# Kernel optimization log

Hardware: AMD Instinct MI355X
Metric: run time of the kernel (lower is better)

Reference implementation:

```python
import jax, jax.numpy as jnp
import numpy as np

D_K = 256.0  # K_dim from __init__, used only as 1/sqrt(d_k) scale


def setup_inputs() -> dict:
    key = jax.random.key(0)
    ks = jax.random.split(key, 8)
    B, S, L, DQ, DK, DV, H = 8, 4096, 64, 1024, 1024, 1024, 256
    Q = jax.random.normal(ks[0], (B, S, DQ), dtype=jnp.float32)
    K = jax.random.normal(ks[1], (L, DK), dtype=jnp.float32)
    V = jax.random.normal(ks[2], (B, S, DV), dtype=jnp.float32)
    attn_mask = jax.random.randint(ks[3], (B, S, 1), 0, 2).astype(jnp.bool_)
    Wq_w = jax.random.normal(ks[4], (H, DQ), dtype=jnp.float32) * 0.02
    Wq_b = jnp.zeros((H,), dtype=jnp.float32)
    Wk_w = jax.random.normal(ks[5], (H, DK), dtype=jnp.float32) * 0.02
    Wk_b = jnp.zeros((H,), dtype=jnp.float32)
    return {"Q": Q, "K": K, "V": V, "attn_mask": attn_mask,
            "Wq_w": Wq_w, "Wq_b": Wq_b, "Wk_w": Wk_w, "Wk_b": Wk_b}


def reference(Q, K, V, attn_mask, Wq_w, Wq_b, Wk_w, Wk_b):
    # Projections (the original's expand/repeat + mul + sum is exactly a GEMM)
    kh = K @ Wk_w.T + Wk_b                                  # (L, 256)
    qh = (Q @ Wq_w.T + Wq_b) / jnp.sqrt(jnp.float32(D_K))   # (B, S, 256)
    # S[b,s,l] = sum_d qh[b,s,d]*kh[l,d]; scores sums over labels too
    S = jnp.einsum('bsd,ld->bsl', qh, kh)                   # (B, S, L)
    scores = S.sum(-1)[..., None] + attn_mask.astype(jnp.float32) * (-1e9)  # (B,S,1)
    scores = jnp.swapaxes(scores, -1, -2)                   # (B, 1, S)
    attn = jax.nn.softmax(scores, axis=-1)                  # (B, 1, S)
    context = jnp.matmul(attn, V)[:, 0, :]                  # (B, DV)
    return context, attn
```

## Files before the change

kernel.cpp:

```cpp
#include <hip/hip_runtime.h>
#include <hip/hip_bf16.h>
#include <cstddef>


#define B 8
#define S 4096
#define DQ 1024
#define H 256
#define L 64
#define SCHUNK 32
#define NSCHUNK (S / SCHUNK)


__global__ void ksumc_kernel(const float* __restrict__ K, float* __restrict__ ks_c) {
    int c = blockIdx.x * 64 + threadIdx.x;
    float acc = 0.f;
#pragma unroll 8
    for (int l = 0; l < L; ++l) acc += K[l * DQ + c];
    ks_c[c] = acc;
}

__global__ void ksum_kernel(const float* __restrict__ Wk_w, const float* __restrict__ Wk_b,
                            const float* __restrict__ ks_c, float* __restrict__ ksum) {
    __shared__ float sv[DQ];
    for (int i = threadIdx.x; i < DQ; i += 256) sv[i] = ks_c[i];
    __syncthreads();
    int wave = threadIdx.x >> 6, lane = threadIdx.x & 63;
    int d = blockIdx.x * 4 + wave;
    const float* wr = Wk_w + (size_t)d * DQ;
    float acc = 0.f;
#pragma unroll
    for (int j = 0; j < 4; ++j) {
        int idx = j * 256 + lane * 4;
        float4 a = *(const float4*)(wr + idx);
        float4 b = *(const float4*)(sv + idx);
        acc += a.x * b.x + a.y * b.y + a.z * b.z + a.w * b.w;
    }
    for (int off = 32; off; off >>= 1) acc += __shfl_down(acc, off);
    if (lane == 0) ksum[d] = acc + 64.f * Wk_b[d];
}

__global__ void wvec_bias_kernel(const float* __restrict__ Wq_w, const float* __restrict__ Wq_b,
                                 const float* __restrict__ ksum, float* __restrict__ w,
                                 float* __restrict__ bias) {
    __shared__ float ks[H];
    __shared__ float red[4][64];
    __shared__ float red2[4];
    ks[threadIdx.x] = ksum[threadIdx.x];
    __syncthreads();
    int wave = threadIdx.x >> 6, lane = threadIdx.x & 63;
    if (blockIdx.x < 16) {
        int c = blockIdx.x * 64 + lane;
        float acc = 0.f;
#pragma unroll 8
        for (int j = 0; j < 64; ++j) {
            int d = wave + 4 * j;
            acc += Wq_w[(size_t)d * DQ + c] * ks[d];
        }
        red[wave][lane] = acc;
        __syncthreads();
        if (wave == 0)
            w[c] = (red[0][lane] + red[1][lane] + red[2][lane] + red[3][lane]) * 0.0625f;
    } else {
        float v = Wq_b[threadIdx.x] * ks[threadIdx.x];
        for (int off = 32; off; off >>= 1) v += __shfl_down(v, off);
        if (lane == 0) red2[wave] = v;
        __syncthreads();
        if (threadIdx.x == 0)
            bias[0] = (red2[0] + red2[1] + red2[2] + red2[3]) * 0.0625f;
    }
}

__global__ void fused_main_kernel(const float* __restrict__ Q, const float* __restrict__ V,
                                  const float* __restrict__ w, const float* __restrict__ bias,
                                  const int* __restrict__ mask,
                                  float* __restrict__ escore, float* __restrict__ partial) {
    int sc = blockIdx.x, b = blockIdx.y;
    __shared__ float sw[DQ];
    __shared__ float es[SCHUNK];
    for (int i = threadIdx.x; i < DQ; i += 256) sw[i] = w[i];
    float sb = bias[0];
    __syncthreads();
    int wave = threadIdx.x >> 6, lane = threadIdx.x & 63;
#pragma unroll
    for (int r = 0; r < 8; ++r) {
        int row = sc * SCHUNK + wave * 8 + r;
        const float* q = Q + ((size_t)b * S + row) * DQ;
        float acc = 0.f;
#pragma unroll
        for (int j = 0; j < 4; ++j) {
            int idx = j * 256 + lane * 4;
            float4 qv = *(const float4*)(q + idx);
            float4 wv = *(const float4*)(sw + idx);
            acc += qv.x * wv.x + qv.y * wv.y + qv.z * wv.z + qv.w * wv.w;
        }
        for (int off = 32; off; off >>= 1) acc += __shfl_down(acc, off);
        if (lane == 0) {
            float e = mask[(size_t)b * S + row] ? 0.f : __expf(acc + sb);
            es[wave * 8 + r] = e;
            escore[(size_t)b * S + row] = e;
        }
    }
    __syncthreads();
    const float* vb = V + ((size_t)b * S + (size_t)sc * SCHUNK) * DQ + threadIdx.x * 4;
    float4 acc4 = {0.f, 0.f, 0.f, 0.f};
#pragma unroll 8
    for (int s = 0; s < SCHUNK; ++s) {
        float a = es[s];
        float4 v = *(const float4*)(vb + (size_t)s * DQ);
        acc4.x += a * v.x; acc4.y += a * v.y; acc4.z += a * v.z; acc4.w += a * v.w;
    }
    *(float4*)(partial + ((size_t)b * NSCHUNK + sc) * DQ + threadIdx.x * 4) = acc4;
}

__global__ void denom_kernel(const float* __restrict__ escore, float* __restrict__ inv) {
    int b = blockIdx.x;
    __shared__ float red[4];
    int wave = threadIdx.x >> 6, lane = threadIdx.x & 63;
    float lsum = 0.f;
    for (int i = threadIdx.x; i < S; i += 256) lsum += escore[(size_t)b * S + i];
    for (int off = 32; off; off >>= 1) lsum += __shfl_down(lsum, off);
    if (lane == 0) red[wave] = lsum;
    __syncthreads();
    if (threadIdx.x == 0) inv[b] = 1.0f / (red[0] + red[1] + red[2] + red[3]);
}

__global__ void epilogue_kernel(const float* __restrict__ escore, const float* __restrict__ partial,
                                const float* __restrict__ inv,
                                float* __restrict__ ctx, float* __restrict__ attn) {
    if (blockIdx.x < 128) {
        int i = blockIdx.x * 256 + threadIdx.x;
        attn[i] = escore[i] * inv[i >> 12];
    } else {
        int idx = (blockIdx.x - 128) * 256 + threadIdx.x;
        int b = idx >> 10, d = idx & 1023;
        const float* p = partial + (size_t)b * NSCHUNK * DQ + d;
        float acc = 0.f;
#pragma unroll 8
        for (int sc = 0; sc < NSCHUNK; ++sc) acc += p[(size_t)sc * DQ];
        ctx[idx] = acc * inv[b];
    }
}

extern "C" void kernel_launch(void* const* d_in, const int* in_sizes, int n_in,
                              void* d_out, int out_size, void* d_ws, size_t ws_size,
                              hipStream_t stream) {
    const float* Q    = (const float*)d_in[0];
    const float* K    = (const float*)d_in[1];
    const float* V    = (const float*)d_in[2];
    const int*   mask = (const int*)d_in[3];
    const float* Wq_w = (const float*)d_in[4];
    const float* Wq_b = (const float*)d_in[5];
    const float* Wk_w = (const float*)d_in[6];
    const float* Wk_b = (const float*)d_in[7];

    float* ws     = (float*)d_ws;
    float* ks_c   = ws;
    float* ksum   = ws + 1024;
    float* wv     = ws + 1280;
    float* bias   = ws + 2304;
    float* inv    = ws + 2312;
    float* escore = ws + 4096;
    float* partial = ws + 4096 + B * S;

    float* ctx  = (float*)d_out;
    float* attn = (float*)d_out + B * DQ;

    ksumc_kernel<<<16, 64, 0, stream>>>(K, ks_c);
    ksum_kernel<<<H / 4, 256, 0, stream>>>(Wk_w, Wk_b, ks_c, ksum);
    wvec_bias_kernel<<<17, 256, 0, stream>>>(Wq_w, Wq_b, ksum, wv, bias);
    fused_main_kernel<<<dim3(NSCHUNK, B), 256, 0, stream>>>(Q, V, wv, bias, mask, escore, partial);
    denom_kernel<<<B, 256, 0, stream>>>(escore, inv);
    epilogue_kernel<<<160, 256, 0, stream>>>(escore, partial, inv, ctx, attn);
}
```

Before: 313.8 us.

## Split fused main kernel into scores and context kernels with atomic denominator

Replaces the fused score-plus-V kernel with two kernels. The first computes masked exp scores for 16 rows per block, issuing all row loads up front with a shared-memory reduction, and accumulates the softmax denominator with atomics, which removes the separate denom kernel. The second reads V in chunks of 16 rows with batched loads to raise memory-level parallelism. The cost is an extra launch, an extra pass over escore, twice as many partial rows for the epilogue to reduce, and a memset.

```diff
diff --git a/kernel.cpp b/kernel.cpp
--- a/kernel.cpp
+++ b/kernel.cpp
@@ -8,8 +8,9 @@
 #define DQ 1024
 #define H 256
 #define L 64
-#define SCHUNK 32
-#define NSCHUNK (S / SCHUNK)
+#define RPB 16
+#define SC2 16
+#define NSC2 (S / SC2)
 
 
 __global__ void ksumc_kernel(const float* __restrict__ K, float* __restrict__ ks_c) {
@@ -71,74 +72,86 @@
     }
 }
 
-__global__ void fused_main_kernel(const float* __restrict__ Q, const float* __restrict__ V,
-                                  const float* __restrict__ w, const float* __restrict__ bias,
-                                  const int* __restrict__ mask,
-                                  float* __restrict__ escore, float* __restrict__ partial) {
-    int sc = blockIdx.x, b = blockIdx.y;
-    __shared__ float sw[DQ];
-    __shared__ float es[SCHUNK];
-    for (int i = threadIdx.x; i < DQ; i += 256) sw[i] = w[i];
-    float sb = bias[0];
+__global__ __launch_bounds__(256) void scores_kernel(
+        const float* __restrict__ Q, const float* __restrict__ w,
+        const float* __restrict__ bias, const int* __restrict__ mask,
+        float* __restrict__ escore, float* __restrict__ denom) {
+    int t = threadIdx.x;
+    size_t base = (size_t)blockIdx.x * RPB;
+    float4 wv = *(const float4*)(w + t * 4);
+    __shared__ float sp[RPB * 256];
+    __shared__ float bsum[RPB];
+    const float* qb = Q + base * DQ + t * 4;
+
+    float4 qv[RPB];
+#pragma unroll
+    for (int r = 0; r < RPB; ++r) qv[r] = *(const float4*)(qb + (size_t)r * DQ);
+#pragma unroll
+    for (int r = 0; r < RPB; ++r)
+        sp[r * 256 + t] = qv[r].x * wv.x + qv[r].y * wv.y + qv[r].z * wv.z + qv[r].w * wv.w;
     __syncthreads();
-    int wave = threadIdx.x >> 6, lane = threadIdx.x & 63;
+
+    int r = t >> 4, j = t & 15;
+    float s = 0.f;
 #pragma unroll
-    for (int r = 0; r < 8; ++r) {
-        int row = sc * SCHUNK + wave * 8 + r;
-        const float* q = Q + ((size_t)b * S + row) * DQ;
-        float acc = 0.f;
+    for (int k = 0; k < 16; ++k) s += sp[r * 256 + k * 16 + j];
+    s += __shfl_xor(s, 8, 64);
+    s += __shfl_xor(s, 4, 64);
+    s += __shfl_xor(s, 2, 64);
+    s += __shfl_xor(s, 1, 64);
+    if (j == 0) {
+        size_t row = base + r;
+        float e = mask[row] ? 0.f : __expf(s + bias[0]);
+        escore[row] = e;
+        bsum[r] = e;
+    }
+    __syncthreads();
+    if (t == 0) {
+        float d0 = 0.f;
 #pragma unroll
-        for (int j = 0; j < 4; ++j) {
-            int idx = j * 256 + lane * 4;
-            float4 qv = *(const float4*)(q + idx);
-            float4 wv = *(const float4*)(sw + idx);
-            acc += qv.x * wv.x + qv.y * wv.y + qv.z * wv.z + qv.w * wv.w;
-        }
-        for (int off = 32; off; off >>= 1) acc += __shfl_down(acc, off);
-        if (lane == 0) {
-            float e = mask[(size_t)b * S + row] ? 0.f : __expf(acc + sb);
-            es[wave * 8 + r] = e;
-            escore[(size_t)b * S + row] = e;
+        for (int k = 0; k < RPB; ++k) d0 += bsum[k];
+        atomicAdd(denom + (base >> 12), d0);
+    }
+}
+
+__global__ __launch_bounds__(256) void ctx_partial_kernel(
+        const float* __restrict__ V, const float* __restrict__ escore,
+        float* __restrict__ partial) {
+    int sc = blockIdx.x, b = blockIdx.y, t = threadIdx.x;
+    __shared__ float es[SC2];
+    if (t < SC2) es[t] = escore[(size_t)b * S + sc * SC2 + t];
+    __syncthreads();
+    const float* vb = V + ((size_t)b * S + (size_t)sc * SC2) * DQ + t * 4;
+    float4 acc = {0.f, 0.f, 0.f, 0.f};
+#pragma unroll
+    for (int s0 = 0; s0 < SC2; s0 += 8) {
+        float4 v[8];
+#pragma unroll
+        for (int k = 0; k < 8; ++k) v[k] = *(const float4*)(vb + (size_t)(s0 + k) * DQ);
+#pragma unroll
+        for (int k = 0; k < 8; ++k) {
+            float a = es[s0 + k];
+            acc.x += a * v[k].x; acc.y += a * v[k].y;
+            acc.z += a * v[k].z; acc.w += a * v[k].w;
         }
     }
-    __syncthreads();
-    const float* vb = V + ((size_t)b * S + (size_t)sc * SCHUNK) * DQ + threadIdx.x * 4;
-    float4 acc4 = {0.f, 0.f, 0.f, 0.f};
-#pragma unroll 8
-    for (int s = 0; s < SCHUNK; ++s) {
-        float a = es[s];
-        float4 v = *(const float4*)(vb + (size_t)s * DQ);
-        acc4.x += a * v.x; acc4.y += a * v.y; acc4.z += a * v.z; acc4.w += a * v.w;
-    }
-    *(float4*)(partial + ((size_t)b * NSCHUNK + sc) * DQ + threadIdx.x * 4) = acc4;
-}
-
-__global__ void denom_kernel(const float* __restrict__ escore, float* __restrict__ inv) {
-    int b = blockIdx.x;
-    __shared__ float red[4];
-    int wave = threadIdx.x >> 6, lane = threadIdx.x & 63;
-    float lsum = 0.f;
-    for (int i = threadIdx.x; i < S; i += 256) lsum += escore[(size_t)b * S + i];
-    for (int off = 32; off; off >>= 1) lsum += __shfl_down(lsum, off);
-    if (lane == 0) red[wave] = lsum;
-    __syncthreads();
-    if (threadIdx.x == 0) inv[b] = 1.0f / (red[0] + red[1] + red[2] + red[3]);
+    *(float4*)(partial + ((size_t)b * NSC2 + sc) * DQ + t * 4) = acc;
 }
 
 __global__ void epilogue_kernel(const float* __restrict__ escore, const float* __restrict__ partial,
-                                const float* __restrict__ inv,
+                                const float* __restrict__ denom,
                                 float* __restrict__ ctx, float* __restrict__ attn) {
     if (blockIdx.x < 128) {
         int i = blockIdx.x * 256 + threadIdx.x;
-        attn[i] = escore[i] * inv[i >> 12];
+        attn[i] = escore[i] / denom[i >> 12];
     } else {
         int idx = (blockIdx.x - 128) * 256 + threadIdx.x;
         int b = idx >> 10, d = idx & 1023;
-        const float* p = partial + (size_t)b * NSCHUNK * DQ + d;
+        const float* p = partial + (size_t)b * NSC2 * DQ + d;
         float acc = 0.f;
 #pragma unroll 8
-        for (int sc = 0; sc < NSCHUNK; ++sc) acc += p[(size_t)sc * DQ];
-        ctx[idx] = acc * inv[b];
+        for (int sc = 0; sc < NSC2; ++sc) acc += p[(size_t)sc * DQ];
+        ctx[idx] = acc / denom[b];
     }
 }
 
@@ -159,17 +172,18 @@
     float* ksum   = ws + 1024;
     float* wv     = ws + 1280;
     float* bias   = ws + 2304;
-    float* inv    = ws + 2312;
+    float* denom  = ws + 2312;
     float* escore = ws + 4096;
     float* partial = ws + 4096 + B * S;
 
     float* ctx  = (float*)d_out;
     float* attn = (float*)d_out + B * DQ;
 
+    hipMemsetAsync(denom, 0, B * sizeof(float), stream);
     ksumc_kernel<<<16, 64, 0, stream>>>(K, ks_c);
     ksum_kernel<<<H / 4, 256, 0, stream>>>(Wk_w, Wk_b, ks_c, ksum);
     wvec_bias_kernel<<<17, 256, 0, stream>>>(Wq_w, Wq_b, ksum, wv, bias);
-    fused_main_kernel<<<dim3(NSCHUNK, B), 256, 0, stream>>>(Q, V, wv, bias, mask, escore, partial);
-    denom_kernel<<<B, 256, 0, stream>>>(escore, inv);
-    epilogue_kernel<<<160, 256, 0, stream>>>(escore, partial, inv, ctx, attn);
+    scores_kernel<<<(B * S) / RPB, 256, 0, stream>>>(Q, wv, bias, mask, escore, denom);
+    ctx_partial_kernel<<<dim3(NSC2, B), 256, 0, stream>>>(V, escore, partial);
+    epilogue_kernel<<<160, 256, 0, stream>>>(escore, partial, denom, ctx, attn);
 }
```

Measured after the change: 323.1 us. 1.03x slower.
